# Optimization experiments

Measured on AMD Instinct MI355X. Metric: run time of the kernel, lower is better.

## Reference

```python
import jax, jax.numpy as jnp
import numpy as np

D_MODEL = 1024
N_HEADS_Q = 16
N_HEADS_KV = 4
D_HEAD = 64  # d_qk = d_v
THETA = 10000.0
CLAMP = 80.0


def apply_rope(x, theta=THETA):
    # x: (b, h, s, d) with d even; interleaved-pair rotary embedding
    b, h, s, d = x.shape
    inv_freq = 1.0 / (theta ** (jnp.arange(0, d, 2, dtype=jnp.float32) / d))  # (d/2,)
    ang = jnp.arange(s, dtype=jnp.float32)[:, None] * inv_freq[None, :]       # (s, d/2)
    cos, sin = jnp.cos(ang), jnp.sin(ang)
    x1, x2 = x[..., 0::2], x[..., 1::2]
    o1 = x1 * cos - x2 * sin
    o2 = x1 * sin + x2 * cos
    return jnp.stack([o1, o2], axis=-1).reshape(b, h, s, d).astype(x.dtype)


def setup_inputs() -> dict:
    key = jax.random.key(0)
    k0, k1, k2, k3, k4 = jax.random.split(key, 5)
    scale = 1.0 / np.sqrt(D_MODEL)
    return {
        "x": jax.random.normal(k0, (2, 2048, D_MODEL), dtype=jnp.float32),
        "Wq": jax.random.normal(k1, (N_HEADS_Q * D_HEAD, D_MODEL), dtype=jnp.float32) * scale,
        "Wk": jax.random.normal(k2, (N_HEADS_KV * D_HEAD, D_MODEL), dtype=jnp.float32) * scale,
        "Wv": jax.random.normal(k3, (N_HEADS_KV * D_HEAD, D_MODEL), dtype=jnp.float32) * scale,
        "Wo": jax.random.normal(k4, (D_MODEL, N_HEADS_Q * D_HEAD), dtype=jnp.float32) * scale,
    }


def _attention(x, Wq, Wk, Wv, Wo):
    b, s, _ = x.shape
    r = N_HEADS_Q // N_HEADS_KV  # queries per KV group
    # projections (Linear: y = x @ W^T, no bias)
    Q = (x @ Wq.T).reshape(b, s, N_HEADS_Q, D_HEAD).transpose(0, 2, 1, 3)   # (b, Hq, s, d)
    K = (x @ Wk.T).reshape(b, s, N_HEADS_KV, D_HEAD).transpose(0, 2, 1, 3)  # (b, Hkv, s, d)
    V = (x @ Wv.T).reshape(b, s, N_HEADS_KV, D_HEAD).transpose(0, 2, 1, 3)
    Q = apply_rope(Q)
    K = apply_rope(K)
    # GQA grouping: (b, Hkv, r, s, d)
    Qg = Q.reshape(b, N_HEADS_KV, r, s, D_HEAD)
    scores = jnp.einsum('bgrqd,bgkd->bgrqk', Qg, K)          # (b, g, r, s, s)
    scores = jnp.clip(scores, -CLAMP, CLAMP)
    causal = jnp.tril(jnp.ones((s, s), dtype=bool))
    scores = jnp.where(causal, scores, -jnp.inf)
    weights = jax.nn.softmax(scores / jnp.sqrt(jnp.float32(D_HEAD)), axis=-1)
    attn = jnp.einsum('bgrqk,bgkd->bgrqd', weights, V)       # (b, g, r, s, d)
    # '... h_kv r s d -> ... s (h_kv r d)'
    attn = attn.transpose(0, 3, 1, 2, 4).reshape(b, s, N_HEADS_Q * D_HEAD)
    return attn @ Wo.T


def reference(x, Wq, Wk, Wv, Wo):
    return _attention(x, Wq, Wk, Wv, Wo)
```

## Files before the change

kernel.cpp:

```cpp
#include <hip/hip_runtime.h>
#include <hip/hip_bf16.h>
#include <math.h>

typedef __attribute__((ext_vector_type(8))) short bf16x8;
typedef __attribute__((ext_vector_type(4))) float f32x4;

#define B_   2
#define S_   2048
#define DM   1024
#define HQ   16
#define HKV  4
#define DH   64

#define MFMA16(a, b, c) __builtin_amdgcn_mfma_f32_16x16x32_bf16(a, b, c, 0, 0, 0)

__device__ __forceinline__ void load_lds16(const __hip_bfloat16* g, __hip_bfloat16* l)
{
    __builtin_amdgcn_global_load_lds(
        (const __attribute__((address_space(1))) unsigned int*)g,
        (__attribute__((address_space(3))) unsigned int*)l, 16, 0, 0);
}

#define CVT_TOTAL 6815744
__global__ void cvt_all(const float* __restrict__ x,  const float* __restrict__ wq,
                        const float* __restrict__ wk, const float* __restrict__ wv,
                        const float* __restrict__ wo,
                        __hip_bfloat16* __restrict__ xb,  __hip_bfloat16* __restrict__ wqb,
                        __hip_bfloat16* __restrict__ wkb, __hip_bfloat16* __restrict__ wvb,
                        __hip_bfloat16* __restrict__ wob)
{
    int i = (blockIdx.x * blockDim.x + threadIdx.x) * 4;
    if (i >= CVT_TOTAL) return;
    const float* src; __hip_bfloat16* dst; int off;
    if      (i < 4194304) { src = x;  dst = xb;  off = 0; }
    else if (i < 5242880) { src = wq; dst = wqb; off = 4194304; }
    else if (i < 5505024) { src = wk; dst = wkb; off = 5242880; }
    else if (i < 5767168) { src = wv; dst = wvb; off = 5505024; }
    else                  { src = wo; dst = wob; off = 5767168; }
    i -= off;
    float4 v = *(const float4*)(src + i);
    union { ushort4 u; __hip_bfloat16 h[4]; } p;
    p.h[0] = __float2bfloat16(v.x);
    p.h[1] = __float2bfloat16(v.y);
    p.h[2] = __float2bfloat16(v.z);
    p.h[3] = __float2bfloat16(v.w);
    *(ushort4*)(dst + i) = p.u;
}

template <bool QKV>
__global__ __launch_bounds__(256, 3) void gemm_tile(
    const __hip_bfloat16* __restrict__ A,
    const __hip_bfloat16* __restrict__ W,
    float* __restrict__ C0, __hip_bfloat16* __restrict__ Qb,
    __hip_bfloat16* __restrict__ Kb, __hip_bfloat16* __restrict__ Vt, int K)
{
    const int wave = threadIdx.x >> 6;
    const int lane = threadIdx.x & 63;
    const int quad = lane >> 4;
    const int l16  = lane & 15;
    const int wm = wave >> 1, wn = wave & 1;
    const int m0 = blockIdx.x * 64;
    const int n0 = blockIdx.y * 128;

    __shared__ __align__(16) __hip_bfloat16 As[64 * 32];
    __shared__ __align__(16) __hip_bfloat16 Bs[128 * 32];

    f32x4 acc[2][4] = {};

    for (int k0 = 0; k0 < K; k0 += 32) {
        #pragma unroll
        for (int r = 0; r < 3; ++r) {
            const int m = wave * 3 + r;
            if (m < 4) {
                const int g = m * 64 + lane;
                const int row = g >> 2;
                const int cbs = ((g & 3) - row) & 3;
                load_lds16(A + (size_t)(m0 + row) * K + k0 + cbs * 8, &As[m * 512]);
            } else {
                const int g = (m - 4) * 64 + lane;
                const int row = g >> 2;
                const int cbs = ((g & 3) - row) & 3;
                load_lds16(W + (size_t)(n0 + row) * K + k0 + cbs * 8, &Bs[(m - 4) * 512]);
            }
        }
        __syncthreads();
        bf16x8 af[2], bf[4];
        #pragma unroll
        for (int i = 0; i < 2; ++i) {
            const int ra = wm * 32 + i * 16 + l16;
            af[i] = *(const bf16x8*)&As[ra * 32 + ((quad + ra) & 3) * 8];
        }
        #pragma unroll
        for (int j = 0; j < 4; ++j) {
            const int rb = wn * 64 + j * 16 + l16;
            bf[j] = *(const bf16x8*)&Bs[rb * 32 + ((quad + rb) & 3) * 8];
        }
        #pragma unroll
        for (int i = 0; i < 2; ++i)
            #pragma unroll
            for (int j = 0; j < 4; ++j)
                acc[i][j] = MFMA16(af[i], bf[j], acc[i][j]);
        __syncthreads();
    }

    #pragma unroll
    for (int j = 0; j < 4; ++j) {
        const int cbase = n0 + wn * 64 + j * 16;
        const int cb = cbase + l16;
        if (QKV && cbase < 1280) {
            const int ii = (cb >> 1) & 31;
            const float f = exp2f((float)ii * -0.41524101186092f);
            const bool odd = cb & 1;
            #pragma unroll
            for (int i = 0; i < 2; ++i) {
                #pragma unroll
                for (int reg = 0; reg < 4; ++reg) {
                    const int row = m0 + wm * 32 + i * 16 + quad * 4 + reg;
                    const float v = acc[i][j][reg];
                    const float p = __shfl_xor(v, 1);
                    const float ang = (float)(row & (S_ - 1)) * f;
                    float sn, cs;
                    sincosf(ang, &sn, &cs);
                    const float o = odd ? (p * sn + v * cs) : (v * cs - p * sn);
                    if (cbase < 1024)
                        Qb[(size_t)row * 1024 + cb] = __float2bfloat16(o);
                    else
                        Kb[(size_t)row * 256 + cb - 1024] = __float2bfloat16(o);
                }
            }
        } else {
            #pragma unroll
            for (int i = 0; i < 2; ++i) {
                #pragma unroll
                for (int reg = 0; reg < 4; ++reg) {
                    const int row = m0 + wm * 32 + i * 16 + quad * 4 + reg;
                    const float v = acc[i][j][reg];
                    if (QKV)
                        Vt[((size_t)(row >> 11) * 256 + (cb - 1280)) * S_ +
                           (row & (S_ - 1))] = __float2bfloat16(v);
                    else
                        C0[(size_t)row * 1024 + cb] = v;
                }
            }
        }
    }
}

__device__ __forceinline__ void softmax_store(
    const f32x4* sacc, int q, int k0, int quad, int l16,
    float& lsum, __hip_bfloat16* PsTile)
{
    #pragma unroll
    for (int nt = 0; nt < 4; ++nt) {
        union { ushort4 u; __hip_bfloat16 h[4]; } pk;
        #pragma unroll
        for (int reg = 0; reg < 4; ++reg) {
            float s = fminf(fmaxf(sacc[nt][reg], -80.0f), 80.0f) * 0.125f;
            float p = __expf(s - 10.0f);
            const int key = k0 + nt * 16 + quad * 4 + reg;
            p = (key <= q) ? p : 0.0f;
            lsum += p;
            pk.h[reg] = __float2bfloat16(p);
        }
        *(ushort4*)&PsTile[l16 * 72 + nt * 16 + quad * 4] = pk.u;
    }
}

__global__ __launch_bounds__(256, 2) void attn_mfma(
    const __hip_bfloat16* __restrict__ Q,
    const __hip_bfloat16* __restrict__ K,
    const __hip_bfloat16* __restrict__ Vt,
    __hip_bfloat16* __restrict__ ctx)
{
    const int t    = blockIdx.x & 15;
    const int hq   = (blockIdx.x >> 4) & (HQ - 1);
    const int b    = blockIdx.x >> 8;
    const int hkv  = hq >> 2;
    const int wave = threadIdx.x >> 6;
    const int lane = threadIdx.x & 63;
    const int quad = lane >> 4;
    const int l16  = lane & 15;

    const int qlo = t * 64 + wave * 16 + l16;
    const int qhi = (31 - t) * 64 + wave * 16 + l16;

    __shared__ __align__(16) __hip_bfloat16 Ks[2][64 * 64];
    __shared__ __align__(16) __hip_bfloat16 Vs[2][64 * 64];
    __shared__ __align__(16) __hip_bfloat16 Ps[4][2][16 * 72];

    const __hip_bfloat16* qpl = Q + ((size_t)(b * S_) + qlo) * (HQ * DH) + hq * DH + quad * 8;
    const __hip_bfloat16* qph = Q + ((size_t)(b * S_) + qhi) * (HQ * DH) + hq * DH + quad * 8;
    bf16x8 ql0 = *(const bf16x8*)qpl;
    bf16x8 ql1 = *(const bf16x8*)(qpl + 32);
    bf16x8 qh0 = *(const bf16x8*)qph;
    bf16x8 qh1 = *(const bf16x8*)(qph + 32);

    const __hip_bfloat16* Kg = K + (size_t)(b * S_) * (HKV * DH) + hkv * DH;
    const __hip_bfloat16* Vg = Vt + (size_t)(b * HKV + hkv) * DH * S_;

    auto stage = [&](int sb, int k0s) {
        #pragma unroll
        for (int r = 0; r < 2; ++r) {
            const int m = wave * 2 + r;
            const int g = m * 64 + lane;
            const int row = g >> 3;
            const int cbs = ((g & 7) - row) & 7;
            load_lds16(Kg + (size_t)(k0s + row) * (HKV * DH) + cbs * 8, &Ks[sb][m * 512]);
            load_lds16(Vg + (size_t)row * S_ + k0s + cbs * 8, &Vs[sb][m * 512]);
        }
    };

    stage(0, 0);

    float lsum_lo = 0.0f, lsum_hi = 0.0f;
    f32x4 Olo[4] = {}, Ohi[4] = {};

    const int last = 31 - t;
    for (int kt = 0; kt <= last; ++kt) {
        const int buf = kt & 1;
        const int k0 = kt * 64;
        __syncthreads();
        if (kt < last) stage(buf ^ 1, k0 + 64);
        const bool dual = (kt <= t);

        bf16x8 ka[4][2];
        #pragma unroll
        for (int nt = 0; nt < 4; ++nt) {
            const int key = nt * 16 + l16;
            ka[nt][0] = *(const bf16x8*)&Ks[buf][key * 64 + ((quad + key) & 7) * 8];
            ka[nt][1] = *(const bf16x8*)&Ks[buf][key * 64 + ((quad + 4 + key) & 7) * 8];
        }
        f32x4 shi[4] = {}, slo[4] = {};
        #pragma unroll
        for (int nt = 0; nt < 4; ++nt) {
            shi[nt] = MFMA16(ka[nt][0], qh0, shi[nt]);
            shi[nt] = MFMA16(ka[nt][1], qh1, shi[nt]);
        }
        if (dual) {
            #pragma unroll
            for (int nt = 0; nt < 4; ++nt) {
                slo[nt] = MFMA16(ka[nt][0], ql0, slo[nt]);
                slo[nt] = MFMA16(ka[nt][1], ql1, slo[nt]);
            }
        }

        softmax_store(shi, qhi, k0, quad, l16, lsum_hi, &Ps[wave][1][0]);
        if (dual) softmax_store(slo, qlo, k0, quad, l16, lsum_lo, &Ps[wave][0][0]);
        __asm__ __volatile__("s_waitcnt lgkmcnt(0)" ::: "memory");

        bf16x8 va[2][4];
        #pragma unroll
        for (int ks = 0; ks < 2; ++ks)
            #pragma unroll
            for (int dt = 0; dt < 4; ++dt) {
                const int d = dt * 16 + l16;
                va[ks][dt] = *(const bf16x8*)
                    &Vs[buf][d * 64 + ((ks * 4 + quad + d) & 7) * 8];
            }
        #pragma unroll
        for (int ks = 0; ks < 2; ++ks) {
            bf16x8 pb = *(const bf16x8*)&Ps[wave][1][l16 * 72 + ks * 32 + quad * 8];
            #pragma unroll
            for (int dt = 0; dt < 4; ++dt)
                Ohi[dt] = MFMA16(va[ks][dt], pb, Ohi[dt]);
        }
        if (dual) {
            #pragma unroll
            for (int ks = 0; ks < 2; ++ks) {
                bf16x8 pb = *(const bf16x8*)&Ps[wave][0][l16 * 72 + ks * 32 + quad * 8];
                #pragma unroll
                for (int dt = 0; dt < 4; ++dt)
                    Olo[dt] = MFMA16(va[ks][dt], pb, Olo[dt]);
            }
        }
    }

    auto finish = [&](float lsum, const f32x4* O, int qrow) {
        lsum += __shfl_xor(lsum, 16);
        lsum += __shfl_xor(lsum, 32);
        const float inv = 1.0f / lsum;
        __hip_bfloat16* cp =
            ctx + ((size_t)(b * S_) + qrow) * (HQ * DH) + hq * DH + quad * 4;
        #pragma unroll
        for (int dt = 0; dt < 4; ++dt) {
            union { ushort4 u; __hip_bfloat16 h[4]; } o;
            #pragma unroll
            for (int reg = 0; reg < 4; ++reg)
                o.h[reg] = __float2bfloat16(O[dt][reg] * inv);
            *(ushort4*)(cp + dt * 16) = o.u;
        }
    };
    finish(lsum_lo, Olo, qlo);
    finish(lsum_hi, Ohi, qhi);
}

extern "C" void kernel_launch(void* const* d_in, const int* in_sizes, int n_in,
                              void* d_out, int out_size, void* d_ws, size_t ws_size,
                              hipStream_t stream)
{
    const float* x  = (const float*)d_in[0];
    const float* Wq = (const float*)d_in[1];
    const float* Wk = (const float*)d_in[2];
    const float* Wv = (const float*)d_in[3];
    const float* Wo = (const float*)d_in[4];
    float* out = (float*)d_out;

    const int M = B_ * S_;

    char* w = (char*)d_ws;
    __hip_bfloat16* xb    = (__hip_bfloat16*)w;  w += (size_t)M * DM * 2;
    __hip_bfloat16* Wqkvb = (__hip_bfloat16*)w;  w += (size_t)1536 * DM * 2;
    __hip_bfloat16* Wob   = (__hip_bfloat16*)w;  w += (size_t)DM * (HQ * DH) * 2;
    __hip_bfloat16* Qb16  = (__hip_bfloat16*)w;  w += (size_t)M * (HQ * DH) * 2;
    __hip_bfloat16* Kb16  = (__hip_bfloat16*)w;  w += (size_t)M * (HKV * DH) * 2;
    __hip_bfloat16* Vt    = (__hip_bfloat16*)w;  w += (size_t)M * (HKV * DH) * 2;
    __hip_bfloat16* ctx   = (__hip_bfloat16*)w;

    __hip_bfloat16* Wqb = Wqkvb;
    __hip_bfloat16* Wkb = Wqkvb + (size_t)1024 * 1024;
    __hip_bfloat16* Wvb = Wqkvb + (size_t)1280 * 1024;

    cvt_all<<<(CVT_TOTAL / 4 + 255) / 256, 256, 0, stream>>>(
        x, Wq, Wk, Wv, Wo, xb, Wqb, Wkb, Wvb, Wob);

    gemm_tile<true><<<dim3(M / 64, 1536 / 128), 256, 0, stream>>>(
        xb, Wqkvb, nullptr, Qb16, Kb16, Vt, DM);

    attn_mfma<<<B_ * HQ * 16, 256, 0, stream>>>(Qb16, Kb16, Vt, ctx);

    gemm_tile<false><<<dim3(M / 64, 1024 / 128), 256, 0, stream>>>(
        ctx, Wob, out, nullptr, nullptr, nullptr, HQ * DH);
}
```

Before: 174.9 us.

## Split paired causal query tiles into separate blocks, skip masking off-diagonal, use hardware sin/cos

The attention kernel stops pairing a low and a high query tile per block and launches one block per 64-row query tile, with the longest tiles dispatched first and occupancy raised to 3 blocks per CU. Causal masking now runs only on the diagonal key tile through a templated softmax. The RoPE epilogue replaces sincosf with range-reduced hardware sin/cos instructions. Together these cut per-block register and LDS pressure and ALU work, but lose the K/V tile reuse between the two query tiles and may slightly reduce RoPE accuracy.

```diff
diff --git a/kernel.cpp b/kernel.cpp
--- a/kernel.cpp
+++ b/kernel.cpp
@@ -110,6 +110,7 @@
         if (QKV && cbase < 1280) {
             const int ii = (cb >> 1) & 31;
             const float f = exp2f((float)ii * -0.41524101186092f);
+            const float f_rev = f * 0.15915494309189535f;
             const bool odd = cb & 1;
             #pragma unroll
             for (int i = 0; i < 2; ++i) {
@@ -118,9 +119,10 @@
                     const int row = m0 + wm * 32 + i * 16 + quad * 4 + reg;
                     const float v = acc[i][j][reg];
                     const float p = __shfl_xor(v, 1);
-                    const float ang = (float)(row & (S_ - 1)) * f;
-                    float sn, cs;
-                    sincosf(ang, &sn, &cs);
+                    float rev = (float)(row & (S_ - 1)) * f_rev;
+                    rev -= floorf(rev);
+                    const float sn = __builtin_amdgcn_sinf(rev);
+                    const float cs = __builtin_amdgcn_cosf(rev);
                     const float o = odd ? (p * sn + v * cs) : (v * cs - p * sn);
                     if (cbase < 1024)
                         Qb[(size_t)row * 1024 + cb] = __float2bfloat16(o);
@@ -146,6 +148,7 @@
     }
 }
 
+template <bool MASKED>
 __device__ __forceinline__ void softmax_store(
     const f32x4* sacc, int q, int k0, int quad, int l16,
     float& lsum, __hip_bfloat16* PsTile)
@@ -157,8 +160,10 @@
         for (int reg = 0; reg < 4; ++reg) {
             float s = fminf(fmaxf(sacc[nt][reg], -80.0f), 80.0f) * 0.125f;
             float p = __expf(s - 10.0f);
-            const int key = k0 + nt * 16 + quad * 4 + reg;
-            p = (key <= q) ? p : 0.0f;
+            if (MASKED) {
+                const int key = k0 + nt * 16 + quad * 4 + reg;
+                p = (key <= q) ? p : 0.0f;
+            }
             lsum += p;
             pk.h[reg] = __float2bfloat16(p);
         }
@@ -166,34 +171,29 @@
     }
 }
 
-__global__ __launch_bounds__(256, 2) void attn_mfma(
+__global__ __launch_bounds__(256, 3) void attn_mfma(
     const __hip_bfloat16* __restrict__ Q,
     const __hip_bfloat16* __restrict__ K,
     const __hip_bfloat16* __restrict__ Vt,
     __hip_bfloat16* __restrict__ ctx)
 {
-    const int t    = blockIdx.x & 15;
-    const int hq   = (blockIdx.x >> 4) & (HQ - 1);
-    const int b    = blockIdx.x >> 8;
+    const int qt   = 31 - (blockIdx.x & 31);
+    const int hq   = (blockIdx.x >> 5) & (HQ - 1);
+    const int b    = blockIdx.x >> 9;
     const int hkv  = hq >> 2;
     const int wave = threadIdx.x >> 6;
     const int lane = threadIdx.x & 63;
     const int quad = lane >> 4;
     const int l16  = lane & 15;
-
-    const int qlo = t * 64 + wave * 16 + l16;
-    const int qhi = (31 - t) * 64 + wave * 16 + l16;
+    const int q    = qt * 64 + wave * 16 + l16;
 
     __shared__ __align__(16) __hip_bfloat16 Ks[2][64 * 64];
     __shared__ __align__(16) __hip_bfloat16 Vs[2][64 * 64];
-    __shared__ __align__(16) __hip_bfloat16 Ps[4][2][16 * 72];
-
-    const __hip_bfloat16* qpl = Q + ((size_t)(b * S_) + qlo) * (HQ * DH) + hq * DH + quad * 8;
-    const __hip_bfloat16* qph = Q + ((size_t)(b * S_) + qhi) * (HQ * DH) + hq * DH + quad * 8;
-    bf16x8 ql0 = *(const bf16x8*)qpl;
-    bf16x8 ql1 = *(const bf16x8*)(qpl + 32);
-    bf16x8 qh0 = *(const bf16x8*)qph;
-    bf16x8 qh1 = *(const bf16x8*)(qph + 32);
+    __shared__ __align__(16) __hip_bfloat16 Ps[4][16 * 72];
+
+    const __hip_bfloat16* qp = Q + ((size_t)(b * S_) + q) * (HQ * DH) + hq * DH + quad * 8;
+    bf16x8 qb0 = *(const bf16x8*)qp;
+    bf16x8 qb1 = *(const bf16x8*)(qp + 32);
 
     const __hip_bfloat16* Kg = K + (size_t)(b * S_) * (HKV * DH) + hkv * DH;
     const __hip_bfloat16* Vg = Vt + (size_t)(b * HKV + hkv) * DH * S_;
@@ -212,16 +212,15 @@
 
     stage(0, 0);
 
-    float lsum_lo = 0.0f, lsum_hi = 0.0f;
-    f32x4 Olo[4] = {}, Ohi[4] = {};
-
-    const int last = 31 - t;
-    for (int kt = 0; kt <= last; ++kt) {
+    float lsum = 0.0f;
+    f32x4 O[4] = {};
+    const f32x4 zro = {0.0f, 0.0f, 0.0f, 0.0f};
+
+    for (int kt = 0; kt <= qt; ++kt) {
         const int buf = kt & 1;
         const int k0 = kt * 64;
         __syncthreads();
-        if (kt < last) stage(buf ^ 1, k0 + 64);
-        const bool dual = (kt <= t);
+        if (kt < qt) stage(buf ^ 1, k0 + 64);
 
         bf16x8 ka[4][2];
         #pragma unroll
@@ -230,22 +229,15 @@
             ka[nt][0] = *(const bf16x8*)&Ks[buf][key * 64 + ((quad + key) & 7) * 8];
             ka[nt][1] = *(const bf16x8*)&Ks[buf][key * 64 + ((quad + 4 + key) & 7) * 8];
         }
-        f32x4 shi[4] = {}, slo[4] = {};
+        f32x4 s[4];
         #pragma unroll
         for (int nt = 0; nt < 4; ++nt) {
-            shi[nt] = MFMA16(ka[nt][0], qh0, shi[nt]);
-            shi[nt] = MFMA16(ka[nt][1], qh1, shi[nt]);
-        }
-        if (dual) {
-            #pragma unroll
-            for (int nt = 0; nt < 4; ++nt) {
-                slo[nt] = MFMA16(ka[nt][0], ql0, slo[nt]);
-                slo[nt] = MFMA16(ka[nt][1], ql1, slo[nt]);
-            }
-        }
-
-        softmax_store(shi, qhi, k0, quad, l16, lsum_hi, &Ps[wave][1][0]);
-        if (dual) softmax_store(slo, qlo, k0, quad, l16, lsum_lo, &Ps[wave][0][0]);
+            s[nt] = MFMA16(ka[nt][0], qb0, zro);
+            s[nt] = MFMA16(ka[nt][1], qb1, s[nt]);
+        }
+
+        if (kt == qt) softmax_store<true >(s, q, k0, quad, l16, lsum, Ps[wave]);
+        else          softmax_store<false>(s, q, k0, quad, l16, lsum, Ps[wave]);
         __asm__ __volatile__("s_waitcnt lgkmcnt(0)" ::: "memory");
 
         bf16x8 va[2][4];
@@ -259,39 +251,25 @@
             }
         #pragma unroll
         for (int ks = 0; ks < 2; ++ks) {
-            bf16x8 pb = *(const bf16x8*)&Ps[wave][1][l16 * 72 + ks * 32 + quad * 8];
+            bf16x8 pb = *(const bf16x8*)&Ps[wave][l16 * 72 + ks * 32 + quad * 8];
             #pragma unroll
             for (int dt = 0; dt < 4; ++dt)
-                Ohi[dt] = MFMA16(va[ks][dt], pb, Ohi[dt]);
-        }
-        if (dual) {
-            #pragma unroll
-            for (int ks = 0; ks < 2; ++ks) {
-                bf16x8 pb = *(const bf16x8*)&Ps[wave][0][l16 * 72 + ks * 32 + quad * 8];
-                #pragma unroll
-                for (int dt = 0; dt < 4; ++dt)
-                    Olo[dt] = MFMA16(va[ks][dt], pb, Olo[dt]);
-            }
-        }
-    }
-
-    auto finish = [&](float lsum, const f32x4* O, int qrow) {
-        lsum += __shfl_xor(lsum, 16);
-        lsum += __shfl_xor(lsum, 32);
-        const float inv = 1.0f / lsum;
-        __hip_bfloat16* cp =
-            ctx + ((size_t)(b * S_) + qrow) * (HQ * DH) + hq * DH + quad * 4;
-        #pragma unroll
-        for (int dt = 0; dt < 4; ++dt) {
-            union { ushort4 u; __hip_bfloat16 h[4]; } o;
-            #pragma unroll
-            for (int reg = 0; reg < 4; ++reg)
-                o.h[reg] = __float2bfloat16(O[dt][reg] * inv);
-            *(ushort4*)(cp + dt * 16) = o.u;
-        }
-    };
-    finish(lsum_lo, Olo, qlo);
-    finish(lsum_hi, Ohi, qhi);
+                O[dt] = MFMA16(va[ks][dt], pb, O[dt]);
+        }
+    }
+
+    lsum += __shfl_xor(lsum, 16);
+    lsum += __shfl_xor(lsum, 32);
+    const float inv = 1.0f / lsum;
+    __hip_bfloat16* cp = ctx + ((size_t)(b * S_) + q) * (HQ * DH) + hq * DH + quad * 4;
+    #pragma unroll
+    for (int dt = 0; dt < 4; ++dt) {
+        union { ushort4 u; __hip_bfloat16 h[4]; } o;
+        #pragma unroll
+        for (int reg = 0; reg < 4; ++reg)
+            o.h[reg] = __float2bfloat16(O[dt][reg] * inv);
+        *(ushort4*)(cp + dt * 16) = o.u;
+    }
 }
 
 extern "C" void kernel_launch(void* const* d_in, const int* in_sizes, int n_in,
@@ -326,7 +304,7 @@
     gemm_tile<true><<<dim3(M / 64, 1536 / 128), 256, 0, stream>>>(
         xb, Wqkvb, nullptr, Qb16, Kb16, Vt, DM);
 
-    attn_mfma<<<B_ * HQ * 16, 256, 0, stream>>>(Qb16, Kb16, Vt, ctx);
+    attn_mfma<<<B_ * HQ * 32, 256, 0, stream>>>(Qb16, Kb16, Vt, ctx);
 
     gemm_tile<false><<<dim3(M / 64, 1024 / 128), 256, 0, stream>>>(
         ctx, Wob, out, nullptr, nullptr, nullptr, HQ * DH);
```

Result: slower. 192.6 us (+10.1%).
